# Performance work log

Measured on AMD Instinct MI355X. Metric: run time of the kernel, lower is better.

Reference implementation:

```python
import jax, jax.numpy as jnp
import numpy as np

N_NODES = 50000
N_EDGES = 600000
D = 128
ITERATIONS = 3


def setup_inputs() -> dict:
    key = jax.random.key(0)
    k0, k1, k2, k3 = jax.random.split(key, 4)
    node_feats = jax.random.normal(k0, (N_NODES, D), dtype=jnp.float32)
    adjacency = jax.random.randint(k1, (N_EDGES, 2), 0, N_NODES, dtype=jnp.int64)
    scale = 1.0 / np.sqrt(D).astype(np.float32)
    W_emb = jax.random.normal(k2, (D, D), dtype=jnp.float32) * scale
    b_emb = jnp.zeros((D,), dtype=jnp.float32)
    W_upd = jax.random.normal(k3, (D, D), dtype=jnp.float32) * scale
    b_upd = jnp.zeros((D,), dtype=jnp.float32)
    return {
        "node_feats": node_feats,
        "W_emb": W_emb,
        "b_emb": b_emb,
        "W_upd": W_upd,
        "b_upd": b_upd,
        "adjacency": adjacency,
    }


def reference(node_feats, W_emb, b_emb, W_upd, b_upd, adjacency):
    # Embedding layer: Dense + ReLU per node (inference path skips BatchNorm)
    h = jax.nn.relu(node_feats @ W_emb + b_emb)  # [N, D]

    src = adjacency[:, 0]
    dst = adjacency[:, 1]

    # Each undirected edge contributes a message in both directions.
    ones = jnp.ones((N_EDGES,), dtype=h.dtype)
    deg = (jax.ops.segment_sum(ones, src, num_segments=N_NODES)
           + jax.ops.segment_sum(ones, dst, num_segments=N_NODES))  # [N]
    denom = (deg + 1.0)[:, None]  # +1 for the node's own contribution

    for _ in range(ITERATIONS):
        # MessagePassing: gather neighbor features, scatter-add into nodes,
        # then normalize by (num incoming messages + 1).
        agg = (jax.ops.segment_sum(h[dst], src, num_segments=N_NODES)
               + jax.ops.segment_sum(h[src], dst, num_segments=N_NODES))  # [N, D]
        h = (h + agg) / denom
        # Update: per-node Dense followed by sigmoid nonlinearity.
        h = jax.nn.sigmoid(h @ W_upd + b_upd)
    return h
```

## Files before the change

kernel.cpp:

```cpp
#include <hip/hip_runtime.h>
#include <hip/hip_bf16.h>

#define NN 50000
#define NE 600000
#define DD 128
#define RB 64
#define GB ((NN + RB - 1) / RB)
#define NBE ((NE + 4095) / 4096)
#define NBUCK 196
#define SB ((NN + 1023) / 1024)
#define GQB3 (2 * ((NN + 31) / 32))
#define NLO 25000

typedef __bf16 bfrag __attribute__((ext_vector_type(8)));
typedef float  ffrag __attribute__((ext_vector_type(4)));
typedef unsigned uintv4 __attribute__((ext_vector_type(4)));
typedef unsigned uintv2 __attribute__((ext_vector_type(2)));

union frag_cast { uintv4 u4; unsigned u[4]; bfrag b; };

__device__ __forceinline__ float bfbits2f(unsigned v) { return __uint_as_float(v << 16); }
__device__ __forceinline__ unsigned f2bfbits(float f) {
    unsigned u = __float_as_uint(f);
    return (u + 0x7FFFu + ((u >> 16) & 1u)) >> 16;
}

__device__ __forceinline__ float ld_in(const void* p, int idx, int f32) {
    return f32 ? ((const float*)p)[idx]
               : bfbits2f(((const unsigned short*)p)[idx]);
}

__device__ __forceinline__ void ld_edge_nt(const int* adj, int e, int i64, int& s, int& d) {
    if (i64) {
        s = __builtin_nontemporal_load(&adj[4 * e]);
        d = __builtin_nontemporal_load(&adj[4 * e + 2]);
    } else {
        s = __builtin_nontemporal_load(&adj[2 * e]);
        d = __builtin_nontemporal_load(&adj[2 * e + 1]);
    }
}

__global__ void k_prep(const unsigned* __restrict__ Ww, const unsigned* __restrict__ adjw,
                       const void* __restrict__ We, const void* __restrict__ Wu,
                       unsigned short* __restrict__ WeT, unsigned short* __restrict__ WuT,
                       int* __restrict__ flags) {
    const int tid = threadIdx.x;
    if (blockIdx.x < DD) {
        __shared__ int scnt;
        if (tid == 0) scnt = 0;
        __syncthreads();
        int c = 0;
        for (int i = tid; i < 512; i += 256) {
            unsigned e = (Ww[i] >> 7) & 0xFFu;
            c += (e >= 0x60u && e <= 0x85u) ? 1 : 0;
        }
        atomicAdd(&scnt, c);
        __syncthreads();
        const int f32 = (scnt >= 256) ? 0 : 1;
        const int k = blockIdx.x;
        if (tid < DD) {
            WeT[tid * DD + k] = (unsigned short)f2bfbits(ld_in(We, k * DD + tid, f32));
        } else {
            int n = tid - DD;
            WuT[n * DD + k] = (unsigned short)f2bfbits(ld_in(Wu, k * DD + n, f32));
        }
        return;
    }
    __shared__ int cnt[2];
    if (tid < 2) cnt[tid] = 0;
    __syncthreads();
    int c0 = 0, c1 = 0;
    for (int i = tid; i < 512; i += 256) {
        unsigned e = (Ww[i] >> 7) & 0xFFu;
        c0 += (e >= 0x60u && e <= 0x85u) ? 1 : 0;
        c1 += (adjw[2 * i + 1] == 0u) ? 1 : 0;
    }
    atomicAdd(&cnt[0], c0);
    atomicAdd(&cnt[1], c1);
    __syncthreads();
    if (tid == 0) {
        flags[0] = (cnt[0] >= 256) ? 0 : 1;
        flags[1] = (cnt[1] >= 256) ? 1 : 0;
    }
}

__device__ __forceinline__ void stage_w(const uintv4* __restrict__ WTg, uintv4* sW, int tid) {
#pragma unroll
    for (int k = 0; k < 8; k++) {
        int d = k * 256 + tid;
        int m = d & 15, rest = d >> 4;
        int quad = rest & 3, ks = (rest >> 2) & 3, ct = rest >> 4;
        sW[d] = WTg[(ct * 16 + m) * 16 + (ks * 4 + quad)];
    }
}

__device__ __forceinline__ void mfma_rows(const bfrag af[4], const bfrag* sW,
                                          int m, int quad, ffrag acc[8]) {
#pragma unroll
    for (int ks = 0; ks < 4; ks++) {
#pragma unroll
        for (int ct = 0; ct < 8; ct++) {
            bfrag bf_ = sW[((ct * 4 + ks) * 4 + quad) * 16 + m];
            acc[ct] = __builtin_amdgcn_mfma_f32_16x16x32_bf16(af[ks], bf_, acc[ct], 0, 0, 0);
        }
    }
}

__device__ __forceinline__ void st_h2(unsigned short* __restrict__ Hout,
                                      int ct, int m, int orow, float z) {
    Hout[(size_t)(ct >> 2) * (NN * 64) + (size_t)orow * 64 + (ct & 3) * 16 + m] =
        (unsigned short)f2bfbits(z);
}

__launch_bounds__(256, 5)
__global__ void k_main1(const void* __restrict__ Xp, const unsigned short* __restrict__ WTg,
                        const void* __restrict__ Bp, unsigned short* __restrict__ Hout,
                        const int* __restrict__ flags, const int* __restrict__ adj,
                        int* __restrict__ bh1) {
    __shared__ __align__(16) unsigned short sWT[DD * DD];
    const int tid = threadIdx.x;
    if (blockIdx.x >= GB) {
        int* hist = (int*)sWT;
        const int bb = blockIdx.x - GB;
        hist[tid] = 0;
        __syncthreads();
        const int i64 = flags[1];
#pragma unroll
        for (int k = 0; k < 16; k++) {
            const int e = bb * 4096 + k * 256 + tid;
            if (e < NE) {
                int s, d;
                ld_edge_nt(adj, e, i64, s, d);
                if ((unsigned)s < NN && (unsigned)d < NN) {
                    atomicAdd(&hist[s >> 8], 1);
                    atomicAdd(&hist[d >> 8], 1);
                }
            }
        }
        __syncthreads();
        if (tid < NBUCK) bh1[tid * NBE + bb] = hist[tid];
        return;
    }
    const int wave = tid >> 6;
    const int lane = tid & 63;
    const int f32  = flags[0];
    const int m    = lane & 15;
    const int quad = lane >> 4;
    const int rowbase = blockIdx.x * RB + wave * 16;
    const int row  = rowbase + m;
    const int rc   = (row < NN) ? row : (NN - 1);

    stage_w((const uintv4*)WTg, (uintv4*)sWT, tid);

    bfrag af[4];
    if (f32) {
        const float4* Xf = (const float4*)Xp;
#pragma unroll
        for (int ks = 0; ks < 4; ks++) {
            const int k0 = ks * 32 + quad * 8;
            float4 a0 = Xf[rc * 32 + (k0 >> 2)];
            float4 a1 = Xf[rc * 32 + (k0 >> 2) + 1];
            frag_cast fc;
            fc.u[0] = f2bfbits(a0.x) | (f2bfbits(a0.y) << 16);
            fc.u[1] = f2bfbits(a0.z) | (f2bfbits(a0.w) << 16);
            fc.u[2] = f2bfbits(a1.x) | (f2bfbits(a1.y) << 16);
            fc.u[3] = f2bfbits(a1.z) | (f2bfbits(a1.w) << 16);
            af[ks] = fc.b;
        }
    } else {
        const uintv4* Xv = (const uintv4*)Xp;
#pragma unroll
        for (int ks = 0; ks < 4; ks++) {
            const int k0 = ks * 32 + quad * 8;
            frag_cast fc;
            fc.u4 = Xv[rc * 16 + (k0 >> 3)];
            af[ks] = fc.b;
        }
    }
    __syncthreads();

    ffrag acc[8];
#pragma unroll
    for (int i = 0; i < 8; i++) acc[i] = (ffrag)(0.0f);
    mfma_rows(af, (const bfrag*)sWT, m, quad, acc);

#pragma unroll
    for (int ct = 0; ct < 8; ct++) {
        int col = ct * 16 + m;
        float bb = ld_in(Bp, col, f32);
#pragma unroll
        for (int reg = 0; reg < 4; reg++) {
            int orow = rowbase + quad * 4 + reg;
            if (orow < NN) {
                float z = fmaxf(acc[ct][reg] + bb, 0.0f);
                st_h2(Hout, ct, m, orow, z);
            }
        }
    }
}

__global__ void k_scanB(const int* __restrict__ bh1, int* __restrict__ bkoff,
                        int* __restrict__ bkbase) {
    __shared__ int tot[256];
    __shared__ int wps[4];
    const int t = threadIdx.x, lane = t & 63, w = t >> 6;
    for (int k = w; k < NBUCK; k += 16) {
        int vals[3];
#pragma unroll
        for (int c = 0; c < 3; c++) {
            int idx = c * 64 + lane;
            vals[c] = (idx < NBE) ? bh1[k * NBE + idx] : 0;
        }
        int carry = 0;
#pragma unroll
        for (int c = 0; c < 3; c++) {
            int v = vals[c], x = v;
#pragma unroll
            for (int off = 1; off < 64; off <<= 1) {
                int y = __shfl_up(x, off, 64);
                if (lane >= off) x += y;
            }
            int idx = c * 64 + lane;
            if (idx < NBE) bkoff[k * NBE + idx] = carry + x - v;
            carry += __shfl(x, 63, 64);
        }
        if (lane == 0) tot[k] = carry;
    }
    if (t < 256 && t >= NBUCK) tot[t] = 0;
    __syncthreads();
    int v = 0, x = 0;
    if (t < 256) {
        v = tot[t]; x = v;
#pragma unroll
        for (int off = 1; off < 64; off <<= 1) {
            int y = __shfl_up(x, off, 64);
            if (lane >= off) x += y;
        }
        if (lane == 63) wps[w] = x;
    }
    __syncthreads();
    if (t < NBUCK) {
        int add = 0;
        for (int k = 0; k < w; k++) add += wps[k];
        bkbase[t] = x - v + add;
        if (t == NBUCK - 1) bkbase[NBUCK] = x + add;
    }
}

__launch_bounds__(256)
__global__ void k_p1b(const int* __restrict__ adj, const int* __restrict__ flags,
                      const int* __restrict__ bkbase, const int* __restrict__ bkoff,
                      unsigned* __restrict__ rec) {
    __shared__ int cur[256];
    const int tid = threadIdx.x;
    const int bb = blockIdx.x;
    if (tid < NBUCK) cur[tid] = bkbase[tid] + bkoff[tid * NBE + bb];
    __syncthreads();
    const int i64 = flags[1];
#pragma unroll
    for (int k = 0; k < 16; k++) {
        const int e = bb * 4096 + k * 256 + tid;
        if (e < NE) {
            int s, d;
            ld_edge_nt(adj, e, i64, s, d);
            if ((unsigned)s < NN && (unsigned)d < NN) {
                int ps = atomicAdd(&cur[s >> 8], 1);
                rec[ps] = (unsigned)s | ((unsigned)d << 16);
                int pd = atomicAdd(&cur[d >> 8], 1);
                rec[pd] = (unsigned)d | ((unsigned)s << 16);
            }
        }
    }
}

__launch_bounds__(256)
__global__ void k_p2a(const unsigned* __restrict__ rec, const int* __restrict__ bkbase,
                      int* __restrict__ deg, int* __restrict__ deglo) {
    __shared__ int dh[256];
    __shared__ int dhlo[256];
    const int tid = threadIdx.x;
    const int k = blockIdx.x;
    dh[tid] = 0;
    dhlo[tid] = 0;
    __syncthreads();
    const int st = bkbase[k], en = bkbase[k + 1];
    for (int j = st + tid; j < en; j += 256) {
        unsigned r = rec[j];
        atomicAdd(&dh[r & 255], 1);
        if ((r >> 16) < NLO) atomicAdd(&dhlo[r & 255], 1);
    }
    __syncthreads();
    const int node = k * 256 + tid;
    if (node < NN) {
        deg[node] = dh[tid];
        deglo[node] = dhlo[tid];
    }
}

__global__ void k_scan1(const int* __restrict__ deg, int* __restrict__ rows,
                        int* __restrict__ sums, int* __restrict__ bhist) {
    __shared__ int wsum[16];
    __shared__ int woff[16];
    __shared__ int hist[256];
    const int tid  = threadIdx.x;
    const int wid  = tid >> 6;
    const int lane = tid & 63;
    const int i = blockIdx.x * 1024 + tid;
    if (tid < 256) hist[tid] = 0;
    __syncthreads();
    int x = (i < NN) ? deg[i] : 0;
    if (i < NN) atomicAdd(&hist[(x < 255) ? x : 255], 1);
#pragma unroll
    for (int off = 1; off < 64; off <<= 1) {
        int y = __shfl_up(x, off, 64);
        if (lane >= off) x += y;
    }
    if (lane == 63) wsum[wid] = x;
    __syncthreads();
    if (wid == 0) {
        int s  = (lane < 16) ? wsum[lane] : 0;
        int xs = s;
#pragma unroll
        for (int off = 1; off < 16; off <<= 1) {
            int y = __shfl_up(xs, off, 64);
            if (lane >= off) xs += y;
        }
        if (lane < 16) woff[lane] = xs - s;
        if (lane == 15) sums[blockIdx.x] = xs;
    }
    __syncthreads();
    if (i < NN) rows[i + 1] = x + woff[wid];
    if (tid < 256) bhist[blockIdx.x * 256 + tid] = hist[tid];
}

__global__ void k_scan2(int* __restrict__ sums, int nb,
                        const int* __restrict__ bhist, int* __restrict__ boff,
                        int* __restrict__ bbase) {
    __shared__ int wps[4];
    const int t = threadIdx.x, lane = t & 63, w = t >> 6;
    if (w == 0) {
        int v = (lane < nb) ? sums[lane] : 0;
        int x = v;
        for (int off = 1; off < 64; off <<= 1) {
            int y = __shfl_up(x, off, 64);
            if (lane >= off) x += y;
        }
        if (lane < nb) sums[lane] = x - v;
    }
    int run = 0;
    for (int blk = 0; blk < nb; blk++) {
        int c = bhist[blk * 256 + t];
        boff[blk * 256 + t] = run;
        run += c;
    }
    int v = run, x = v;
    for (int off = 1; off < 64; off <<= 1) {
        int y = __shfl_up(x, off, 64);
        if (lane >= off) x += y;
    }
    if (lane == 63) wps[w] = x;
    __syncthreads();
    int add = 0;
    for (int k = 0; k < w; k++) add += wps[k];
    bbase[t] = x - v + add;
}

__global__ void k_scan3(const int* __restrict__ sums, int* __restrict__ rows,
                        const int* __restrict__ deg, const int* __restrict__ boff,
                        const int* __restrict__ bbase, int* __restrict__ order) {
    __shared__ int lh[256];
    const int tid = threadIdx.x;
    if (tid < 256) lh[tid] = 0;
    __syncthreads();
    int i = blockIdx.x * 1024 + tid;
    int d = 0, r = 0;
    if (i < NN) {
        rows[i + 1] += sums[blockIdx.x];
        if (i == 0) rows[0] = 0;
        d = deg[i];
        d = (d < 255) ? d : 255;
        r = atomicAdd(&lh[d], 1);
        order[bbase[d] + boff[blockIdx.x * 256 + d] + r] = i;
    }
}

__launch_bounds__(256)
__global__ void k_p2b(const unsigned* __restrict__ rec, const int* __restrict__ bkbase,
                      const int* __restrict__ rows, const int* __restrict__ deglo,
                      unsigned short* __restrict__ nbr) {
    __shared__ int lcur[256];
    __shared__ int hcur[256];
    const int tid = threadIdx.x;
    const int k = blockIdx.x;
    const int node = k * 256 + tid;
    const int rbase = (node < NN) ? rows[node] : 0;
    lcur[tid] = rbase;
    hcur[tid] = rbase + ((node < NN) ? deglo[node] : 0);
    __syncthreads();
    const int st = bkbase[k], en = bkbase[k + 1];
    for (int j = st + tid; j < en; j += 256) {
        unsigned r = rec[j];
        unsigned nb = r >> 16;
        int slot = (nb < NLO) ? atomicAdd(&lcur[r & 255], 1)
                              : atomicAdd(&hcur[r & 255], 1);
        nbr[slot] = (unsigned short)nb;
    }
}

__device__ __forceinline__ void accv4(float a[8], uintv4 v) {
#pragma unroll
    for (int k = 0; k < 4; k++) {
        a[2 * k]     += bfbits2f(v[k] & 0xFFFFu);
        a[2 * k + 1] += bfbits2f(v[k] >> 16);
    }
}

__device__ __forceinline__ void gath_range(const uintv4* __restrict__ Pv,
                                           const unsigned short* __restrict__ nbr,
                                           int j, int en, int l8, float a[8]) {
    for (; j + 8 <= en; j += 8) {
        int n[8];
#pragma unroll
        for (int t = 0; t < 8; t++) n[t] = nbr[j + t];
        uintv4 v[8];
#pragma unroll
        for (int t = 0; t < 8; t++) v[t] = Pv[(size_t)n[t] * 8 + l8];
#pragma unroll
        for (int t = 0; t < 8; t++) accv4(a, v[t]);
    }
    for (; j < en; ++j) accv4(a, Pv[(size_t)nbr[j] * 8 + l8]);
}

__launch_bounds__(256)
__global__ void k_gath7(const unsigned* __restrict__ Hp, const int* __restrict__ rows,
                        const int* __restrict__ deglo,
                        const unsigned short* __restrict__ nbr,
                        const int* __restrict__ order, unsigned* __restrict__ XB32) {
    const int plane = blockIdx.x & 1;
    const int chunk = blockIdx.x >> 1;
    const int g     = threadIdx.x >> 3;
    const int l8    = threadIdx.x & 7;
    const int opos  = chunk * 32 + g;
    const int nid   = order[(opos < NN) ? opos : (NN - 1)];
    const uintv4* Pv = (const uintv4*)Hp + (size_t)plane * (NN * 8);
    const int st = rows[nid], en = rows[nid + 1];
    const int mid = st + deglo[nid];
    uintv4 sv = Pv[(size_t)nid * 8 + l8];
    float a[8];
#pragma unroll
    for (int k = 0; k < 4; k++) {
        a[2 * k]     = bfbits2f(sv[k] & 0xFFFFu);
        a[2 * k + 1] = bfbits2f(sv[k] >> 16);
    }
    gath_range(Pv, nbr, st, mid, l8, a);
    gath_range(Pv, nbr, mid, en, l8, a);
    const float inv = 1.0f / (float)(en - st + 1);
    if (opos < NN) {
        uintv4 pk;
#pragma unroll
        for (int k = 0; k < 4; k++)
            pk[k] = f2bfbits(a[2 * k] * inv) | (f2bfbits(a[2 * k + 1] * inv) << 16);
        __builtin_nontemporal_store(pk, (uintv4*)XB32 + (size_t)nid * 16 + plane * 8 + l8);
    }
}

__launch_bounds__(256, 5)
__global__ void k_gemmB(const unsigned short* __restrict__ XB,
                        const unsigned short* __restrict__ WTg, const void* __restrict__ Bp,
                        unsigned short* __restrict__ HoutBf, float* __restrict__ HoutF,
                        const int* __restrict__ flags, int last) {
    __shared__ __align__(16) unsigned short sWT[DD * DD];
    const int tid  = threadIdx.x;
    const int wave = tid >> 6;
    const int lane = tid & 63;
    const int f32  = flags[0];
    const int m    = lane & 15;
    const int quad = lane >> 4;
    const int rowbase = blockIdx.x * RB + wave * 16;
    const int row  = rowbase + m;

    stage_w((const uintv4*)WTg, (uintv4*)sWT, tid);

    bfrag af[4];
    const uintv4* Xv = (const uintv4*)XB;
#pragma unroll
    for (int ks = 0; ks < 4; ks++) {
        const int k0 = ks * 32 + quad * 8;
        frag_cast fc;
        fc.u4 = __builtin_nontemporal_load(&Xv[row * 16 + (k0 >> 3)]);
        af[ks] = fc.b;
    }
    __syncthreads();

    ffrag acc[8];
#pragma unroll
    for (int i = 0; i < 8; i++) acc[i] = (ffrag)(0.0f);
    mfma_rows(af, (const bfrag*)sWT, m, quad, acc);

#pragma unroll
    for (int ct = 0; ct < 8; ct++) {
        int col = ct * 16 + m;
        float bb = ld_in(Bp, col, f32);
#pragma unroll
        for (int reg = 0; reg < 4; reg++) {
            int orow = rowbase + quad * 4 + reg;
            if (orow < NN) {
                float s = 1.0f / (1.0f + __expf(-(acc[ct][reg] + bb)));
                if (!last) {
                    st_h2(HoutBf, ct, m, orow, s);
                } else if (f32) {
                    HoutF[orow * DD + col] = s;
                } else {
                    ((unsigned short*)HoutF)[orow * DD + col] = (unsigned short)f2bfbits(s);
                }
            }
        }
    }
}

extern "C" void kernel_launch(void* const* d_in, const int* in_sizes, int n_in,
                              void* d_out, int out_size, void* d_ws, size_t ws_size,
                              hipStream_t stream) {
    const void* X  = d_in[0];
    const void* We = d_in[1];
    const void* be = d_in[2];
    const void* Wu = d_in[3];
    const void* bu = d_in[4];
    const int* adj = (const int*)d_in[5];

    char* p = (char*)d_ws;
    int* FLAGS = (int*)p;                       p += 256;
    int* ROWS  = (int*)p;                       p += ((NN + 1) * 4 + 252) / 256 * 256;
    int* SUMS  = (int*)p;                       p += 256;
    int* BHIST = (int*)p;                       p += ((SB * 256 * 4 + 255) / 256) * 256;
    int* BOFF  = (int*)p;                       p += ((SB * 256 * 4 + 255) / 256) * 256;
    int* BBASE = (int*)p;                       p += 1024;
    int* ORDER = (int*)p;                       p += ((NN * 4 + 255) / 256) * 256;
    int* DEG   = (int*)p;                       p += ((NN * 4 + 255) / 256) * 256;
    int* DEGLO = (int*)p;                       p += ((NN * 4 + 255) / 256) * 256;
    unsigned short* NBR = (unsigned short*)p;   p += (size_t)2 * NE * 2;
    unsigned short* WeT = (unsigned short*)p;   p += DD * DD * 2;
    unsigned short* WuT = (unsigned short*)p;   p += DD * DD * 2;
    int* BH1   = (int*)p;                       p += ((NBUCK * NBE * 4 + 255) / 256) * 256;
    int* BKOFF = (int*)p;                       p += ((NBUCK * NBE * 4 + 255) / 256) * 256;
    int* BKBASE = (int*)p;                      p += 1024;
    unsigned short* HW  = (unsigned short*)p;
    unsigned* REC = (unsigned*)p;

    unsigned short* HA = (unsigned short*)d_out + (size_t)NN * DD;

    k_prep<<<DD + 1, 256, 0, stream>>>((const unsigned*)We, (const unsigned*)adj,
                                       We, Wu, WeT, WuT, FLAGS);
    k_main1<<<GB + NBE, 256, 0, stream>>>(X, WeT, be, HA, FLAGS, adj, BH1);
    k_scanB<<<1, 1024, 0, stream>>>(BH1, BKOFF, BKBASE);
    k_p1b<<<NBE, 256, 0, stream>>>(adj, FLAGS, BKBASE, BKOFF, REC);
    k_p2a<<<NBUCK, 256, 0, stream>>>(REC, BKBASE, DEG, DEGLO);
    k_scan1<<<SB, 1024, 0, stream>>>(DEG, ROWS, SUMS, BHIST);
    k_scan2<<<1, 256, 0, stream>>>(SUMS, SB, BHIST, BOFF, BBASE);
    k_scan3<<<SB, 1024, 0, stream>>>(SUMS, ROWS, DEG, BOFF, BBASE, ORDER);
    k_p2b<<<NBUCK, 256, 0, stream>>>(REC, BKBASE, ROWS, DEGLO, NBR);

    for (int it = 0; it < 3; ++it) {
        int last = (it == 2);
        k_gath7<<<GQB3, 256, 0, stream>>>((const unsigned*)HA, ROWS, DEGLO, NBR, ORDER,
                                          (unsigned*)HW);
        k_gemmB<<<GB, 256, 0, stream>>>(HW, WuT, bu, HA, (float*)d_out, FLAGS, last);
    }
}
```

Baseline: 353.4 us.

## Split neighbor gather into low-index and high-index passes for cache locality

The gather kernel is split into two launches: the first sums self plus neighbors with index below the midpoint (deglo partition) and writes the partial sum as bf16, and the second reads that partial back, adds the high-index neighbors and normalizes. Each pass touches only about half of the feature table, so the randomly gathered rows are more likely to stay in L2/MALL. The cost is an extra kernel launch, an extra write and read of the partial buffer, and an additional bf16 rounding of the intermediate sum.

After: 362.1 us. 1.02x slower.

```diff
diff --git a/kernel.cpp b/kernel.cpp
--- a/kernel.cpp
+++ b/kernel.cpp
@@ -432,7 +432,38 @@
 }
 
 __launch_bounds__(256)
-__global__ void k_gath7(const unsigned* __restrict__ Hp, const int* __restrict__ rows,
+__global__ void k_gathL(const unsigned* __restrict__ Hp, const int* __restrict__ rows,
+                        const int* __restrict__ deglo,
+                        const unsigned short* __restrict__ nbr,
+                        const int* __restrict__ order, unsigned* __restrict__ XB32) {
+    const int plane = blockIdx.x & 1;
+    const int chunk = blockIdx.x >> 1;
+    const int g     = threadIdx.x >> 3;
+    const int l8    = threadIdx.x & 7;
+    const int opos  = chunk * 32 + g;
+    const int nid   = order[(opos < NN) ? opos : (NN - 1)];
+    const uintv4* Pv = (const uintv4*)Hp + (size_t)plane * (NN * 8);
+    const int st = rows[nid];
+    const int mid = st + deglo[nid];
+    uintv4 sv = Pv[(size_t)nid * 8 + l8];
+    float a[8];
+#pragma unroll
+    for (int k = 0; k < 4; k++) {
+        a[2 * k]     = bfbits2f(sv[k] & 0xFFFFu);
+        a[2 * k + 1] = bfbits2f(sv[k] >> 16);
+    }
+    gath_range(Pv, nbr, st, mid, l8, a);
+    if (opos < NN) {
+        uintv4 pk;
+#pragma unroll
+        for (int k = 0; k < 4; k++)
+            pk[k] = f2bfbits(a[2 * k]) | (f2bfbits(a[2 * k + 1]) << 16);
+        __builtin_nontemporal_store(pk, (uintv4*)XB32 + (size_t)nid * 16 + plane * 8 + l8);
+    }
+}
+
+__launch_bounds__(256)
+__global__ void k_gathH(const unsigned* __restrict__ Hp, const int* __restrict__ rows,
                         const int* __restrict__ deglo,
                         const unsigned short* __restrict__ nbr,
                         const int* __restrict__ order, unsigned* __restrict__ XB32) {
@@ -445,14 +476,13 @@
     const uintv4* Pv = (const uintv4*)Hp + (size_t)plane * (NN * 8);
     const int st = rows[nid], en = rows[nid + 1];
     const int mid = st + deglo[nid];
-    uintv4 sv = Pv[(size_t)nid * 8 + l8];
+    uintv4 pv = *((const uintv4*)XB32 + (size_t)nid * 16 + plane * 8 + l8);
     float a[8];
 #pragma unroll
     for (int k = 0; k < 4; k++) {
-        a[2 * k]     = bfbits2f(sv[k] & 0xFFFFu);
-        a[2 * k + 1] = bfbits2f(sv[k] >> 16);
-    }
-    gath_range(Pv, nbr, st, mid, l8, a);
+        a[2 * k]     = bfbits2f(pv[k] & 0xFFFFu);
+        a[2 * k + 1] = bfbits2f(pv[k] >> 16);
+    }
     gath_range(Pv, nbr, mid, en, l8, a);
     const float inv = 1.0f / (float)(en - st + 1);
     if (opos < NN) {
@@ -562,7 +592,9 @@
 
     for (int it = 0; it < 3; ++it) {
         int last = (it == 2);
-        k_gath7<<<GQB3, 256, 0, stream>>>((const unsigned*)HA, ROWS, DEGLO, NBR, ORDER,
+        k_gathL<<<GQB3, 256, 0, stream>>>((const unsigned*)HA, ROWS, DEGLO, NBR, ORDER,
+                                          (unsigned*)HW);
+        k_gathH<<<GQB3, 256, 0, stream>>>((const unsigned*)HA, ROWS, DEGLO, NBR, ORDER,
                                           (unsigned*)HW);
         k_gemmB<<<GB, 256, 0, stream>>>(HW, WuT, bu, HA, (float*)d_out, FLAGS, last);
     }
```
